# Kernel tuning notes

Hardware: AMD Instinct MI355X
Metric: run time of the kernel (lower is better)

The kernel has to match this reference:

```python
import jax, jax.numpy as jnp
import numpy as np

R = 10000   # relation_num
E = 256     # emb_size == hidden_size
B = 1024    # batch
L = 8       # body length (loop runs L-1 steps)


def setup_inputs() -> dict:
    key = jax.random.key(0)
    ks = jax.random.split(key, 10)
    s = 0.05
    return {
        "bodys": jax.random.randint(ks[0], (B, L), 0, R),
        "emb_w": jax.random.normal(ks[1], (R, E), jnp.float32) * s,
        "w_ih": jax.random.normal(ks[2], (4 * E, E), jnp.float32) * s,
        "w_hh": jax.random.normal(ks[3], (4 * E, E), jnp.float32) * s,
        "b_ih": jax.random.normal(ks[4], (4 * E,), jnp.float32) * s,
        "b_hh": jax.random.normal(ks[5], (4 * E,), jnp.float32) * s,
        "fc1_w": jax.random.normal(ks[6], (E, 2 * E), jnp.float32) * s,
        "fc1_b": jax.random.normal(ks[7], (E,), jnp.float32) * s,
        "fc2_w": jax.random.normal(ks[8], (R + 1, E), jnp.float32) * s,
        "fc2_b": jax.random.normal(ks[9], (R + 1,), jnp.float32) * s,
    }


def _lstm(x, w_ih, w_hh, b_ih, b_hh):
    # x: [B, L, E] -> hidden states [B, L, H] (torch gate order i,f,g,o)
    Bn, _, H = x.shape[0], x.shape[1], w_hh.shape[1]
    h0 = jnp.zeros((Bn, H), x.dtype)
    c0 = jnp.zeros((Bn, H), x.dtype)

    def step(carry, xt):
        h, c = carry
        g = xt @ w_ih.T + b_ih + h @ w_hh.T + b_hh
        i, f, gg, o = jnp.split(g, 4, axis=-1)
        c = jax.nn.sigmoid(f) * c + jax.nn.sigmoid(i) * jnp.tanh(gg)
        h = jax.nn.sigmoid(o) * jnp.tanh(c)
        return (h, c), h

    _, hs = jax.lax.scan(step, (h0, c0), x.transpose(1, 0, 2))
    return hs.transpose(1, 0, 2)


def reference(bodys, emb_w, w_ih, w_hh, b_ih, b_hh, fc1_w, fc1_b, fc2_w, fc2_b):
    x = emb_w[bodys]                       # [B, L, E] embedded body relations
    body_hid = _lstm(x, w_ih, w_hh, b_ih, b_hh)  # [B, L, E]
    Rn = emb_w.shape[0]
    prob = emb_concat = prob_sf = None
    for i in range(body_hid.shape[1] - 1):   # short fixed unroll (L-1 steps)
        if i == 0:
            emb_1 = x[:, 0, :]
            second = x[:, 1, :]
        else:
            # prob_sf @ cat(embedding(indices), body_hid[:, i])  without [B,R+1,E]
            emb_1 = prob_sf[:, :Rn] @ emb_w + prob_sf[:, Rn:] * body_hid[:, i, :]
            # relation_emb[:, i+1, :] == emb_w[i+1] broadcast over batch
            second = jnp.broadcast_to(emb_w[i + 1], emb_1.shape)
        emb_concat = jnp.concatenate([emb_1, second], axis=1)   # [B, 2E]
        prob = jax.nn.relu(emb_concat @ fc1_w.T + fc1_b) @ fc2_w.T + fc2_b  # [B, R+1]
        prob_sf = jax.nn.softmax(prob, axis=1)
    return prob, emb_concat
```

## Files before the change

kernel.cpp:

```cpp
#include <hip/hip_runtime.h>

#define Bv 1024
#define Ev 256
#define Lv 8
#define Rv 10000
#define NP1 10001
#define PS2 10240
#define NPAD 10112
#define BM 64
#define BN 128
#define NSLICE 16
#define NSLOT 158
#define RPSTRIDE 160

typedef __attribute__((ext_vector_type(8))) short bf16x8;
typedef __attribute__((ext_vector_type(4))) float f32x4;

__device__ __forceinline__ float b2f(unsigned short u) {
    union { unsigned int i; float f; } v; v.i = ((unsigned int)u) << 16; return v.f;
}
__device__ __forceinline__ unsigned short f2b(float f) {
    union { float f; unsigned int i; } v; v.f = f;
    unsigned int r = v.i + 0x7fffu + ((v.i >> 16) & 1u);
    return (unsigned short)(r >> 16);
}
__device__ __forceinline__ void glds16(const void* g, void* l) {
    __builtin_amdgcn_global_load_lds(
        (const __attribute__((address_space(1))) void*)g,
        (__attribute__((address_space(3))) void*)l, 16, 0, 0);
}

__global__ __launch_bounds__(256) void gemm_tile(
    const unsigned short* __restrict__ A1, int lda1,
    const unsigned short* __restrict__ W1, int ldw1,
    const float* __restrict__ bias1,
    int Ktot, int kchunk, int Ncols, int mode,
    float* __restrict__ outF, unsigned short* __restrict__ outB, int ldc,
    float* __restrict__ rowPart, float* __restrict__ sfLastU)
{
    __shared__ unsigned short As[2][BM * 32];
    __shared__ unsigned short Bs[2][BN * 32];

    int bmode = mode & 7;
    int swz   = mode >> 4;
    int bx, by, bz;
    if (swz == 1) {
        int r = blockIdx.x & 7, q = blockIdx.x >> 3;
        bx = q & 15; by = r + (q >> 4) * 8; bz = 0;
        if (by >= NPAD / BN) return;
    } else if (swz == 2) {
        int r = blockIdx.x & 7, q = blockIdx.x >> 3;
        bz = r + (q >> 5) * 8; bx = (q & 31) >> 1; by = q & 1;
    } else {
        bx = blockIdx.x; by = blockIdx.y; bz = blockIdx.z;
    }

    int tid  = threadIdx.x;
    int wave = tid >> 6;
    int lane = tid & 63;
    int quad = lane >> 4;
    int l16  = lane & 15;
    int wm = (wave & 1) * 32;
    int wn = (wave >> 1) * 64;
    int m0 = bx * BM;
    int n0 = by * BN;
    int k0 = bz * kchunk;
    int k1 = k0 + kchunk; if (k1 > Ktot) k1 = Ktot;

    f32x4 acc[2][4];
#pragma unroll
    for (int i = 0; i < 2; ++i)
#pragma unroll
        for (int j = 0; j < 4; ++j) acc[i][j] = (f32x4){0.f, 0.f, 0.f, 0.f};

    int c0 = tid, c1 = 256 + tid;
    int row0 = c0 >> 2, row1 = c1 >> 2;
    int g80 = ((c0 & 3) ^ (row0 & 3) ^ ((row0 >> 2) & 3)) * 8;
    int g81 = ((c1 & 3) ^ (row1 & 3) ^ ((row1 >> 2) & 3)) * 8;

    bool first = true;
    for (int k = k0; k < k1; k += 64) {
        if (!first) __syncthreads();
        first = false;
#pragma unroll
        for (int h = 0; h < 2; ++h) {
            int kk = k + h * 32;
            glds16(A1 + (size_t)(m0 + row0) * lda1 + kk + g80, As[h] + (wave * 64) * 8);
            glds16(W1 + (size_t)(n0 + row0) * ldw1 + kk + g80, Bs[h] + (wave * 64) * 8);
            glds16(W1 + (size_t)(n0 + row1) * ldw1 + kk + g81, Bs[h] + (256 + wave * 64) * 8);
        }
        asm volatile("s_waitcnt vmcnt(0)" ::: "memory");
        __syncthreads();

#pragma unroll
        for (int h = 0; h < 2; ++h) {
            bf16x8 af[2], bfr[4];
#pragma unroll
            for (int t = 0; t < 2; ++t) {
                int m = wm + t * 16 + l16;
                int ca = quad ^ (m & 3) ^ ((m >> 2) & 3);
                af[t] = *(const bf16x8*)(As[h] + m * 32 + ca * 8);
            }
#pragma unroll
            for (int t = 0; t < 4; ++t) {
                int n = wn + t * 16 + l16;
                int cb = quad ^ (n & 3) ^ ((n >> 2) & 3);
                bfr[t] = *(const bf16x8*)(Bs[h] + n * 32 + cb * 8);
            }
#pragma unroll
            for (int i = 0; i < 2; ++i)
#pragma unroll
                for (int j = 0; j < 4; ++j)
                    acc[i][j] = __builtin_amdgcn_mfma_f32_16x16x32_bf16(
                        af[i], bfr[j], acc[i][j], 0, 0, 0);
        }
    }

    if (bmode == 5) {
        float rsum[2][4];
#pragma unroll
        for (int i = 0; i < 2; ++i)
#pragma unroll
            for (int r = 0; r < 4; ++r) rsum[i][r] = 0.f;
#pragma unroll
        for (int j = 0; j < 4; ++j) {
            int n = n0 + wn + j * 16 + l16;
            bool valid = (n < Ncols);
            float bsum = valid ? bias1[n] : 0.f;
#pragma unroll
            for (int i = 0; i < 2; ++i) {
                int mBase = m0 + wm + i * 16 + quad * 4;
#pragma unroll
                for (int r = 0; r < 4; ++r) {
                    float e = 0.f;
                    unsigned short w = 0;
                    if (valid) {
                        e = expf(acc[i][j][r] + bsum);
                        w = f2b(e);
                        if (n == Rv) sfLastU[mBase + r] = e;
                    }
                    outB[(size_t)(mBase + r) * ldc + n] = w;
                    rsum[i][r] += e;
                }
            }
        }
        int slot = by * 2 + (wn >> 6);
#pragma unroll
        for (int i = 0; i < 2; ++i)
#pragma unroll
            for (int r = 0; r < 4; ++r) {
                float s = rsum[i][r];
                s += __shfl_xor(s, 1);
                s += __shfl_xor(s, 2);
                s += __shfl_xor(s, 4);
                s += __shfl_xor(s, 8);
                if (l16 == 0) {
                    int m = m0 + wm + i * 16 + quad * 4 + r;
                    rowPart[(size_t)m * RPSTRIDE + slot] = s;
                }
            }
        return;
    }

#pragma unroll
    for (int j = 0; j < 4; ++j) {
        int n = n0 + wn + j * 16 + l16;
        if (n >= Ncols) continue;
        float bsum = bias1 ? bias1[n] : 0.f;
#pragma unroll
        for (int i = 0; i < 2; ++i) {
            int mBase = m0 + wm + i * 16 + quad * 4;
#pragma unroll
            for (int r = 0; r < 4; ++r) {
                float v = acc[i][j][r] + bsum;
                size_t idx = (size_t)(mBase + r) * ldc + n;
                if (bmode == 0)      outF[idx] = v;
                else                 outF[(size_t)bz * (Bv * Ev) + idx] = v;
            }
        }
    }
}

__global__ __launch_bounds__(256) void gemm64(
    const unsigned short* __restrict__ A1, int lda1,
    const unsigned short* __restrict__ W1, int ldw1,
    const unsigned short* __restrict__ A2, int lda2,
    const unsigned short* __restrict__ W2, int ldw2,
    const float* __restrict__ bias1,
    int Ktot, int Ncols, int mode,
    float* __restrict__ outF, unsigned short* __restrict__ outB,
    int ldc, int nshift)
{
    __shared__ unsigned short As[2][64 * 32];
    __shared__ unsigned short Bs[2][64 * 32];

    int bmode = mode & 7;
    int bx = blockIdx.x >> nshift;
    int by = blockIdx.x & ((1 << nshift) - 1);
    int tid  = threadIdx.x;
    int wave = tid >> 6;
    int lane = tid & 63;
    int quad = lane >> 4;
    int l16  = lane & 15;
    int m0 = bx * 64;
    int n0 = by * 64;

    f32x4 acc[4];
#pragma unroll
    for (int j = 0; j < 4; ++j) acc[j] = (f32x4){0.f, 0.f, 0.f, 0.f};

    int row = tid >> 2;
    int g8  = ((tid & 3) ^ (row & 3) ^ ((row >> 2) & 3)) * 8;

    int nSrc = A2 ? 2 : 1;
    bool first = true;
    for (int s = 0; s < nSrc; ++s) {
        const unsigned short* A = s ? A2 : A1; int lda = s ? lda2 : lda1;
        const unsigned short* W = s ? W2 : W1; int ldw = s ? ldw2 : ldw1;
        for (int k = 0; k < Ktot; k += 64) {
            if (!first) __syncthreads();
            first = false;
#pragma unroll
            for (int h = 0; h < 2; ++h) {
                int kk = k + h * 32;
                glds16(A + (size_t)(m0 + row) * lda + kk + g8, As[h] + wave * 512);
                glds16(W + (size_t)(n0 + row) * ldw + kk + g8, Bs[h] + wave * 512);
            }
            asm volatile("s_waitcnt vmcnt(0)" ::: "memory");
            __syncthreads();

#pragma unroll
            for (int h = 0; h < 2; ++h) {
                int ml = wave * 16 + l16;
                int ca = quad ^ (ml & 3) ^ ((ml >> 2) & 3);
                bf16x8 a = *(const bf16x8*)(As[h] + ml * 32 + ca * 8);
#pragma unroll
                for (int j = 0; j < 4; ++j) {
                    int nl = j * 16 + l16;
                    int cb = quad ^ (nl & 3) ^ ((nl >> 2) & 3);
                    bf16x8 b = *(const bf16x8*)(Bs[h] + nl * 32 + cb * 8);
                    acc[j] = __builtin_amdgcn_mfma_f32_16x16x32_bf16(a, b, acc[j], 0, 0, 0);
                }
            }
        }
    }

    if (bmode == 4) {
        int e  = by * 16 + l16;
        float bi = bias1[n0 + l16];
        float bf_ = bias1[n0 + 16 + l16];
        float bg = bias1[n0 + 32 + l16];
        float bo = bias1[n0 + 48 + l16];
#pragma unroll
        for (int r = 0; r < 4; ++r) {
            int m = m0 + wave * 16 + quad * 4 + r;
            float gi = acc[0][r] + bi;
            float gf = acc[1][r] + bf_;
            float gg = acc[2][r] + bg;
            float go = acc[3][r] + bo;
            float cp = (mode & 8) ? 0.f : outF[(size_t)m * 256 + e];
            float si = 1.f / (1.f + expf(-gi));
            float sf = 1.f / (1.f + expf(-gf));
            float so = 1.f / (1.f + expf(-go));
            float cn = sf * cp + si * tanhf(gg);
            outF[(size_t)m * 256 + e] = cn;
            outB[(size_t)m * 256 + e] = f2b(so * tanhf(cn));
        }
        return;
    }

#pragma unroll
    for (int j = 0; j < 4; ++j) {
        int n = n0 + j * 16 + l16;
        if (n >= Ncols) continue;
        float bsum = bias1 ? bias1[n] : 0.f;
#pragma unroll
        for (int r = 0; r < 4; ++r) {
            int m = m0 + wave * 16 + quad * 4 + r;
            float v = acc[j][r] + bsum;
            if (bmode == 1) outB[(size_t)m * ldc + n] = f2b(v > 0.f ? v : 0.f);
            else            outB[(size_t)m * ldc + n] = f2b(v);
        }
    }
}

__global__ void prep_k(const float* __restrict__ w_ih,
                       const float* __restrict__ w_hh,
                       const float* __restrict__ fc1_w,
                       const float* __restrict__ fc2_w,
                       const float* __restrict__ b_ih,
                       const float* __restrict__ b_hh,
                       const int* __restrict__ bodys,
                       const float* __restrict__ emb_w,
                       unsigned short* __restrict__ w_ih_b,
                       unsigned short* __restrict__ w_hh_b,
                       unsigned short* __restrict__ fc1_w_b,
                       unsigned short* __restrict__ fc2_w_b,
                       float* __restrict__ biasC,
                       unsigned short* __restrict__ x,
                       unsigned short* __restrict__ embT,
                       unsigned short* __restrict__ embc,
                       unsigned short* __restrict__ sfA)
{
    __shared__ float tile[32][33];
    int b = blockIdx.x, t = threadIdx.x;
    if (b < 1264) {
#pragma unroll
        for (int j = 0; j < 8; ++j) {
            int i = b * 2048 + j * 256 + t;
            fc2_w_b[i] = (i < NP1 * Ev) ? f2b(fc2_w[i]) : (unsigned short)0;
        }
    } else if (b < 1520) {
        int bb = b - 1264;
        const float* src = (bb < 128) ? w_ih : w_hh;
        unsigned short* dst = (bb < 128) ? w_ih_b : w_hh_b;
        int rb = (bb & 127) * 8;
#pragma unroll
        for (int j = 0; j < 8; ++j) {
            int r = rb + j;
            int gate = (r >> 4) & 3;
            int e = (r & 15) | ((r >> 6) << 4);
            dst[(size_t)r * 256 + t] = f2b(src[(size_t)(gate * 256 + e) * 256 + t]);
        }
    } else if (b < 1584) {
        int base = (b - 1520) * 2048;
#pragma unroll
        for (int j = 0; j < 8; ++j) {
            int i = base + j * 256 + t;
            fc1_w_b[i] = f2b(fc1_w[i]);
        }
    } else if (b < 1585) {
#pragma unroll
        for (int j = 0; j < 4; ++j) {
            int r = j * 256 + t;
            int gate = (r >> 4) & 3;
            int e = (r & 15) | ((r >> 6) << 4);
            biasC[r] = b_ih[gate * 256 + e] + b_hh[gate * 256 + e];
        }
    } else if (b < 2609) {
        int bb = b - 1585;
#pragma unroll
        for (int j = 0; j < 8; ++j) {
            int row = bb * 8 + j;
            x[(size_t)row * Ev + t] = f2b(emb_w[(size_t)bodys[row] * Ev + t]);
        }
    } else if (b < 5169) {
        int bb = b - 2609;
        int kt = (bb % 320) * 32, et = (bb / 320) * 32;
        int tx = t & 31, ty = t >> 5;
#pragma unroll
        for (int r = ty; r < 32; r += 8) {
            int k = kt + r;
            tile[r][tx] = (k < Rv) ? emb_w[(size_t)k * Ev + et + tx] : 0.f;
        }
        __syncthreads();
#pragma unroll
        for (int r = ty; r < 32; r += 8) {
            embT[(size_t)(et + r) * PS2 + kt + tx] = f2b(tile[tx][r]);
        }
    } else {
        int bb = b - 5169;
        embc[(size_t)bb * 512 + t]       = f2b(emb_w[(size_t)bodys[bb * Lv + 0] * Ev + t]);
        embc[(size_t)bb * 512 + 256 + t] = f2b(emb_w[(size_t)bodys[bb * Lv + 1] * Ev + t]);
        if (t < PS2 - NPAD) sfA[(size_t)bb * PS2 + NPAD + t] = 0;
    }
}

__global__ void finalize_emb(const float* __restrict__ emb1p,
                             const float* __restrict__ rowPart,
                             const float* __restrict__ sfLastU,
                             const unsigned short* __restrict__ h_i,
                             const float* __restrict__ emb_row,
                             unsigned short* __restrict__ embc,
                             float* __restrict__ outTail)
{
    int b = blockIdx.x, e = threadIdx.x;
    int wave = e >> 6, lane = e & 63;
    __shared__ float sred[4];
    float ps = (e < NSLOT) ? rowPart[(size_t)b * RPSTRIDE + e] : 0.f;
    for (int off = 32; off; off >>= 1) ps += __shfl_down(ps, off);
    if (lane == 0) sred[wave] = ps;
    __syncthreads();
    float inv = 1.f / (sred[0] + sred[1] + sred[2] + sred[3]);

    float v = 0.f;
#pragma unroll
    for (int z = 0; z < NSLICE; ++z)
        v += emb1p[(size_t)z * (Bv * Ev) + (size_t)b * Ev + e];
    v += sfLastU[b] * b2f(h_i[(size_t)b * Ev + e]);
    v *= inv;
    float w = emb_row[e];
    embc[(size_t)b * 512 + e]       = f2b(v);
    embc[(size_t)b * 512 + 256 + e] = f2b(w);
    if (outTail) {
        outTail[(size_t)b * 512 + e]       = v;
        outTail[(size_t)b * 512 + 256 + e] = w;
    }
}

extern "C" void kernel_launch(void* const* d_in, const int* in_sizes, int n_in,
                              void* d_out, int out_size, void* d_ws, size_t ws_size,
                              hipStream_t stream)
{
    const int*   bodys = (const int*)d_in[0];
    const float* emb_w = (const float*)d_in[1];
    const float* w_ih  = (const float*)d_in[2];
    const float* w_hh  = (const float*)d_in[3];
    const float* b_ih  = (const float*)d_in[4];
    const float* b_hh  = (const float*)d_in[5];
    const float* fc1_w = (const float*)d_in[6];
    const float* fc1_b = (const float*)d_in[7];
    const float* fc2_w = (const float*)d_in[8];
    const float* fc2_b = (const float*)d_in[9];
    float* out = (float*)d_out;

    char* ws = (char*)d_ws;
    size_t off = 0;
    auto alloc = [&](size_t bytes) -> void* {
        void* p = ws + off;
        off += (bytes + 255) & ~(size_t)255;
        return p;
    };
    unsigned short* x       = (unsigned short*)alloc((size_t)Bv * Lv * Ev * 2);
    unsigned short* hs      = (unsigned short*)alloc((size_t)Lv * Bv * Ev * 2);
    float*          cbuf    = (float*)alloc((size_t)Bv * Ev * 4);
    unsigned short* embT    = (unsigned short*)alloc((size_t)Ev * PS2 * 2);
    unsigned short* sfA     = (unsigned short*)alloc((size_t)Bv * PS2 * 2);
    float*          sfLastU = (float*)alloc((size_t)Bv * 4);
    float*          rowPart = (float*)alloc((size_t)Bv * RPSTRIDE * 4);
    float*          emb1p   = (float*)alloc((size_t)NSLICE * Bv * Ev * 4);
    unsigned short* embc    = (unsigned short*)alloc((size_t)Bv * 512 * 2);
    unsigned short* hiddenA = (unsigned short*)alloc((size_t)Bv * Ev * 2);
    unsigned short* w_ih_b  = (unsigned short*)alloc((size_t)1024 * Ev * 2);
    unsigned short* w_hh_b  = (unsigned short*)alloc((size_t)1024 * Ev * 2);
    float*          biasC   = (float*)alloc((size_t)1024 * 4);
    unsigned short* fc1_w_b = (unsigned short*)alloc((size_t)Ev * 512 * 2);
    unsigned short* fc2_w_b = (unsigned short*)alloc((size_t)NPAD * Ev * 2);
    (void)ws_size; (void)in_sizes; (void)n_in; (void)out_size;

    prep_k<<<6193, 256, 0, stream>>>(w_ih, w_hh, fc1_w, fc2_w, b_ih, b_hh,
                                     bodys, emb_w,
                                     w_ih_b, w_hh_b, fc1_w_b, fc2_w_b, biasC, x,
                                     embT, embc, sfA);

    for (int t = 0; t < Lv; ++t) {
        gemm64<<<256, 256, 0, stream>>>(
            x + t * Ev, Lv * Ev, w_ih_b, Ev,
            (t == 0) ? nullptr : (hs + (size_t)(t - 1) * Bv * Ev), Ev, w_hh_b, Ev,
            biasC,
            Ev, 1024, 4 | (t == 0 ? 8 : 0),
            cbuf, hs + (size_t)t * Bv * Ev, 1024, 4);
    }

    for (int i = 0; i < 7; ++i) {
        if (i > 0) {
            gemm_tile<<<512, 256, 0, stream>>>(
                sfA, PS2, embT, PS2,
                nullptr,
                PS2, PS2 / NSLICE, Ev, 2 | (2 << 4),
                emb1p, nullptr, Ev, nullptr, nullptr);
            finalize_emb<<<Bv, 256, 0, stream>>>(
                emb1p, rowPart, sfLastU, hs + (size_t)i * Bv * Ev,
                emb_w + (size_t)(i + 1) * Ev, embc,
                (i == 6) ? (out + (size_t)Bv * NP1) : nullptr);
        }
        gemm64<<<64, 256, 0, stream>>>(
            embc, 512, fc1_w_b, 512, nullptr, 0, nullptr, 0,
            fc1_b,
            512, 256, 1,
            nullptr, hiddenA, 256, 2);
        if (i < 6) {
            gemm_tile<<<1280, 256, 0, stream>>>(
                hiddenA, Ev, fc2_w_b, Ev,
                fc2_b,
                Ev, Ev, NP1, 5 | (1 << 4),
                nullptr, sfA, PS2, rowPart, sfLastU);
        } else {
            gemm_tile<<<1280, 256, 0, stream>>>(
                hiddenA, Ev, fc2_w_b, Ev,
                fc2_b,
                Ev, Ev, NP1, 0 | (1 << 4),
                out, nullptr, NP1, nullptr, nullptr);
        }
    }
}
```

Before: 472.6 us.

## Precompute LSTM input projections in one GEMM and store split-K partials as bf16

The input-to-hidden projection for all timesteps is now computed once by a single large GEMM into an fp32 buffer. Each recurrent step then multiplies only h by w_hh and adds the precomputed gate values in its epilogue, halving per-step K and dropping the input GEMM from the serial chain. The split-K partials of the softmax-times-embedding product are also written as bf16 instead of fp32, halving that intermediate traffic at some accuracy cost. The added xg buffer costs 32 MB of extra writes and reads. The t=0 step now runs with K=0.

After: 456.5 us. 3.4% less time.

```diff
diff --git a/kernel.cpp b/kernel.cpp
--- a/kernel.cpp
+++ b/kernel.cpp
@@ -175,7 +175,7 @@
                 float v = acc[i][j][r] + bsum;
                 size_t idx = (size_t)(mBase + r) * ldc + n;
                 if (bmode == 0)      outF[idx] = v;
-                else                 outF[(size_t)bz * (Bv * Ev) + idx] = v;
+                else                 outB[(size_t)bz * (Bv * Ev) + idx] = f2b(v);
             }
         }
     }
@@ -184,12 +184,11 @@
 __global__ __launch_bounds__(256) void gemm64(
     const unsigned short* __restrict__ A1, int lda1,
     const unsigned short* __restrict__ W1, int ldw1,
-    const unsigned short* __restrict__ A2, int lda2,
-    const unsigned short* __restrict__ W2, int ldw2,
     const float* __restrict__ bias1,
     int Ktot, int Ncols, int mode,
     float* __restrict__ outF, unsigned short* __restrict__ outB,
-    int ldc, int nshift)
+    int ldc, int nshift,
+    const float* __restrict__ xgate, int tstep)
 {
     __shared__ unsigned short As[2][64 * 32];
     __shared__ unsigned short Bs[2][64 * 32];
@@ -212,35 +211,30 @@
     int row = tid >> 2;
     int g8  = ((tid & 3) ^ (row & 3) ^ ((row >> 2) & 3)) * 8;
 
-    int nSrc = A2 ? 2 : 1;
     bool first = true;
-    for (int s = 0; s < nSrc; ++s) {
-        const unsigned short* A = s ? A2 : A1; int lda = s ? lda2 : lda1;
-        const unsigned short* W = s ? W2 : W1; int ldw = s ? ldw2 : ldw1;
-        for (int k = 0; k < Ktot; k += 64) {
-            if (!first) __syncthreads();
-            first = false;
-#pragma unroll
-            for (int h = 0; h < 2; ++h) {
-                int kk = k + h * 32;
-                glds16(A + (size_t)(m0 + row) * lda + kk + g8, As[h] + wave * 512);
-                glds16(W + (size_t)(n0 + row) * ldw + kk + g8, Bs[h] + wave * 512);
-            }
-            asm volatile("s_waitcnt vmcnt(0)" ::: "memory");
-            __syncthreads();
-
-#pragma unroll
-            for (int h = 0; h < 2; ++h) {
-                int ml = wave * 16 + l16;
-                int ca = quad ^ (ml & 3) ^ ((ml >> 2) & 3);
-                bf16x8 a = *(const bf16x8*)(As[h] + ml * 32 + ca * 8);
-#pragma unroll
-                for (int j = 0; j < 4; ++j) {
-                    int nl = j * 16 + l16;
-                    int cb = quad ^ (nl & 3) ^ ((nl >> 2) & 3);
-                    bf16x8 b = *(const bf16x8*)(Bs[h] + nl * 32 + cb * 8);
-                    acc[j] = __builtin_amdgcn_mfma_f32_16x16x32_bf16(a, b, acc[j], 0, 0, 0);
-                }
+    for (int k = 0; k < Ktot; k += 64) {
+        if (!first) __syncthreads();
+        first = false;
+#pragma unroll
+        for (int h = 0; h < 2; ++h) {
+            int kk = k + h * 32;
+            glds16(A1 + (size_t)(m0 + row) * lda1 + kk + g8, As[h] + wave * 512);
+            glds16(W1 + (size_t)(n0 + row) * ldw1 + kk + g8, Bs[h] + wave * 512);
+        }
+        asm volatile("s_waitcnt vmcnt(0)" ::: "memory");
+        __syncthreads();
+
+#pragma unroll
+        for (int h = 0; h < 2; ++h) {
+            int ml = wave * 16 + l16;
+            int ca = quad ^ (ml & 3) ^ ((ml >> 2) & 3);
+            bf16x8 a = *(const bf16x8*)(As[h] + ml * 32 + ca * 8);
+#pragma unroll
+            for (int j = 0; j < 4; ++j) {
+                int nl = j * 16 + l16;
+                int cb = quad ^ (nl & 3) ^ ((nl >> 2) & 3);
+                bf16x8 b = *(const bf16x8*)(Bs[h] + nl * 32 + cb * 8);
+                acc[j] = __builtin_amdgcn_mfma_f32_16x16x32_bf16(a, b, acc[j], 0, 0, 0);
             }
         }
     }
@@ -254,10 +248,11 @@
 #pragma unroll
         for (int r = 0; r < 4; ++r) {
             int m = m0 + wave * 16 + quad * 4 + r;
-            float gi = acc[0][r] + bi;
-            float gf = acc[1][r] + bf_;
-            float gg = acc[2][r] + bg;
-            float go = acc[3][r] + bo;
+            const float* xr = xgate + ((size_t)m * Lv + tstep) * 1024 + n0 + l16;
+            float gi = acc[0][r] + bi + xr[0];
+            float gf = acc[1][r] + bf_ + xr[16];
+            float gg = acc[2][r] + bg + xr[32];
+            float go = acc[3][r] + bo + xr[48];
             float cp = (mode & 8) ? 0.f : outF[(size_t)m * 256 + e];
             float si = 1.f / (1.f + expf(-gi));
             float sf = 1.f / (1.f + expf(-gf));
@@ -366,7 +361,7 @@
     }
 }
 
-__global__ void finalize_emb(const float* __restrict__ emb1p,
+__global__ void finalize_emb(const unsigned short* __restrict__ emb1p,
                              const float* __restrict__ rowPart,
                              const float* __restrict__ sfLastU,
                              const unsigned short* __restrict__ h_i,
@@ -386,7 +381,7 @@
     float v = 0.f;
 #pragma unroll
     for (int z = 0; z < NSLICE; ++z)
-        v += emb1p[(size_t)z * (Bv * Ev) + (size_t)b * Ev + e];
+        v += b2f(emb1p[(size_t)z * (Bv * Ev) + (size_t)b * Ev + e]);
     v += sfLastU[b] * b2f(h_i[(size_t)b * Ev + e]);
     v *= inv;
     float w = emb_row[e];
@@ -424,11 +419,12 @@
     unsigned short* x       = (unsigned short*)alloc((size_t)Bv * Lv * Ev * 2);
     unsigned short* hs      = (unsigned short*)alloc((size_t)Lv * Bv * Ev * 2);
     float*          cbuf    = (float*)alloc((size_t)Bv * Ev * 4);
+    float*          xg      = (float*)alloc((size_t)Bv * Lv * 1024 * 4);
     unsigned short* embT    = (unsigned short*)alloc((size_t)Ev * PS2 * 2);
     unsigned short* sfA     = (unsigned short*)alloc((size_t)Bv * PS2 * 2);
     float*          sfLastU = (float*)alloc((size_t)Bv * 4);
     float*          rowPart = (float*)alloc((size_t)Bv * RPSTRIDE * 4);
-    float*          emb1p   = (float*)alloc((size_t)NSLICE * Bv * Ev * 4);
+    unsigned short* emb1p   = (unsigned short*)alloc((size_t)NSLICE * Bv * Ev * 2);
     unsigned short* embc    = (unsigned short*)alloc((size_t)Bv * 512 * 2);
     unsigned short* hiddenA = (unsigned short*)alloc((size_t)Bv * Ev * 2);
     unsigned short* w_ih_b  = (unsigned short*)alloc((size_t)1024 * Ev * 2);
@@ -443,13 +439,19 @@
                                      w_ih_b, w_hh_b, fc1_w_b, fc2_w_b, biasC, x,
                                      embT, embc, sfA);
 
+    gemm_tile<<<dim3(128, 8, 1), 256, 0, stream>>>(
+        x, Ev, w_ih_b, Ev,
+        nullptr,
+        Ev, Ev, 1024, 0,
+        xg, nullptr, 1024, nullptr, nullptr);
+
     for (int t = 0; t < Lv; ++t) {
         gemm64<<<256, 256, 0, stream>>>(
-            x + t * Ev, Lv * Ev, w_ih_b, Ev,
-            (t == 0) ? nullptr : (hs + (size_t)(t - 1) * Bv * Ev), Ev, w_hh_b, Ev,
+            hs + (size_t)(t ? t - 1 : 0) * Bv * Ev, Ev, w_hh_b, Ev,
             biasC,
-            Ev, 1024, 4 | (t == 0 ? 8 : 0),
-            cbuf, hs + (size_t)t * Bv * Ev, 1024, 4);
+            (t == 0) ? 0 : Ev, 1024, 4 | (t == 0 ? 8 : 0),
+            cbuf, hs + (size_t)t * Bv * Ev, 1024, 4,
+            xg, t);
     }
 
     for (int i = 0; i < 7; ++i) {
@@ -458,17 +460,18 @@
                 sfA, PS2, embT, PS2,
                 nullptr,
                 PS2, PS2 / NSLICE, Ev, 2 | (2 << 4),
-                emb1p, nullptr, Ev, nullptr, nullptr);
+                nullptr, emb1p, Ev, nullptr, nullptr);
             finalize_emb<<<Bv, 256, 0, stream>>>(
                 emb1p, rowPart, sfLastU, hs + (size_t)i * Bv * Ev,
                 emb_w + (size_t)(i + 1) * Ev, embc,
                 (i == 6) ? (out + (size_t)Bv * NP1) : nullptr);
         }
         gemm64<<<64, 256, 0, stream>>>(
-            embc, 512, fc1_w_b, 512, nullptr, 0, nullptr, 0,
+            embc, 512, fc1_w_b, 512,
             fc1_b,
             512, 256, 1,
-            nullptr, hiddenA, 256, 2);
+            nullptr, hiddenA, 256, 2,
+            nullptr, 0);
         if (i < 6) {
             gemm_tile<<<1280, 256, 0, stream>>>(
                 hiddenA, Ev, fc2_w_b, Ev,
```
